# Performance work log

Hardware: AMD Instinct MI355X
Metric: run time of the kernel (lower is better)

Reference implementation:

```python
import jax, jax.numpy as jnp
import numpy as np

B = 4096          # batch
F = 1024          # feature_count * embedding_dim
E = 16            # embedding_dim (domain embedding)
D = 8             # num_domains
T = F + E         # cross-net total dim
L = 3             # cross layers
EPS = 1e-5


def setup_inputs() -> dict:
    key = jax.random.key(0)
    ks = jax.random.split(key, 32)
    s = 0.02
    inp = {}
    inp["x"] = jax.random.normal(ks[0], (B, F), dtype=jnp.float32)
    inp["domain_ids"] = jax.random.randint(ks[1], (B,), 0, D)
    # partitioned normalization params
    inp["pn_weight"] = jnp.ones((D, F), jnp.float32)
    inp["pn_bias"] = jnp.zeros((D, F), jnp.float32)
    # domain embedding table
    inp["dom_emb"] = jax.random.normal(ks[2], (D, E), jnp.float32) * 0.1
    # cross network: L layers, each Linear(T->1, no bias) + additive bias vector
    inp["cross_w"] = jax.random.normal(ks[3], (L, T), jnp.float32) * s
    inp["cross_b"] = jnp.zeros((L, T), jnp.float32)
    # center MLP: T->512->256->128 (ReLU, ReLU, none)
    inp["cW1"] = jax.random.normal(ks[4], (T, 512), jnp.float32) * s
    inp["cb1"] = jnp.zeros((512,), jnp.float32)
    inp["cW2"] = jax.random.normal(ks[5], (512, 256), jnp.float32) * s
    inp["cb2"] = jnp.zeros((256,), jnp.float32)
    inp["cW3"] = jax.random.normal(ks[6], (256, 128), jnp.float32) * s
    inp["cb3"] = jnp.zeros((128,), jnp.float32)
    # per-domain nets: T->512->256->128; last bias initialized to domain_net_init_bias=1.0
    inp["dW1"] = jax.random.normal(ks[7], (D, T, 512), jnp.float32) * s
    inp["db1"] = jnp.zeros((D, 512), jnp.float32)
    inp["dW2"] = jax.random.normal(ks[8], (D, 512, 256), jnp.float32) * s
    inp["db2"] = jnp.zeros((D, 256), jnp.float32)
    inp["dW3"] = jax.random.normal(ks[9], (D, 256, 128), jnp.float32) * s
    inp["db3"] = jnp.ones((D, 128), jnp.float32)
    # final MLP: 128->64->1
    inp["fW1"] = jax.random.normal(ks[10], (128, 64), jnp.float32) * s
    inp["fb1"] = jnp.zeros((64,), jnp.float32)
    inp["fW2"] = jax.random.normal(ks[11], (64, 1), jnp.float32) * s
    inp["fb2"] = jnp.zeros((1,), jnp.float32)
    # auxiliary net: E->32->1
    inp["aW1"] = jax.random.normal(ks[12], (E, 32), jnp.float32) * s
    inp["ab1"] = jnp.zeros((32,), jnp.float32)
    inp["aW2"] = jax.random.normal(ks[13], (32, 1), jnp.float32) * s
    inp["ab2"] = jnp.zeros((1,), jnp.float32)
    return inp


def _forward(x, domain_ids, pn_weight, pn_bias, dom_emb, cross_w, cross_b,
             cW1, cb1, cW2, cb2, cW3, cb3,
             dW1, db1, dW2, db2, dW3, db3,
             fW1, fb1, fW2, fb2, aW1, ab1, aW2, ab2):
    # --- PartitionedNormalization: per-sample LayerNorm stats + domain-indexed affine ---
    mean = jnp.mean(x, axis=1, keepdims=True)
    var = jnp.mean((x - mean) ** 2, axis=1, keepdims=True)  # unbiased=False
    normed = (x - mean) / jnp.sqrt(var + EPS)
    normed = normed * pn_weight[domain_ids] + pn_bias[domain_ids]

    xd = dom_emb[domain_ids]                    # (B, E)
    x0 = jnp.concatenate([normed, xd], axis=1)  # (B, T)

    # --- CrossNetworkWithDomain ---
    xc = x0
    for i in range(L):
        proj = xc @ cross_w[i]                  # (B,)
        xc = x0 * proj[:, None] + cross_b[i] + xc

    # --- center MLP ---
    h = jax.nn.relu(xc @ cW1 + cb1)
    h = jax.nn.relu(h @ cW2 + cb2)
    h_center = h @ cW3 + cb3                    # (B, 128)

    # --- domain-specific nets: run all D nets, select per-sample ---
    a = jax.nn.relu(jnp.einsum('bi,dio->bdo', xc, dW1) + db1[None])   # (B, D, 512)
    a = jax.nn.relu(jnp.einsum('bdi,dio->bdo', a, dW2) + db2[None])   # (B, D, 256)
    a = jnp.einsum('bdi,dio->bdo', a, dW3) + db3[None]                # (B, D, 128)
    h_domain = a[jnp.arange(a.shape[0]), domain_ids]                  # (B, 128)

    # --- STAR fusion (tanh) ---
    fused = h_center * jnp.tanh(h_domain)

    # --- final MLP + auxiliary net ---
    main_logits = jax.nn.relu(fused @ fW1 + fb1) @ fW2 + fb2          # (B, 1)
    aux_logits = jax.nn.relu(xd @ aW1 + ab1) @ aW2 + ab2              # (B, 1)
    return jax.nn.sigmoid(main_logits + aux_logits)


def reference(x, domain_ids, pn_weight, pn_bias, dom_emb, cross_w, cross_b,
              cW1, cb1, cW2, cb2, cW3, cb3,
              dW1, db1, dW2, db2, dW3, db3,
              fW1, fb1, fW2, fb2, aW1, ab1, aW2, ab2):
    return _forward(x, domain_ids, pn_weight, pn_bias, dom_emb, cross_w, cross_b,
                    cW1, cb1, cW2, cb2, cW3, cb3,
                    dW1, db1, dW2, db2, dW3, db3,
                    fW1, fb1, fW2, fb2, aW1, ab1, aW2, ab2)
```

## Files before the change

kernel.cpp:

```cpp
#include <hip/hip_runtime.h>
#include <math.h>
#include <stdint.h>

#define BATCH 4096
#define FEAT  1024
#define EDIM  16
#define NDOM  8
#define TDIM  1040
#define KP1   1088
#define NLAYER 3
#define EPSV  1e-5f

typedef __attribute__((ext_vector_type(8))) short bf16x8;
typedef __attribute__((ext_vector_type(4))) float f32x4;

__device__ __forceinline__ unsigned short f2bf(float f) {
    union { float f; unsigned int u; } v; v.f = f;
    unsigned int u = v.u;
    return (unsigned short)((u + 0x7fffu + ((u >> 16) & 1u)) >> 16);
}
__device__ __forceinline__ float bf2f(unsigned short u) {
    union { unsigned int u; float f; } v; v.u = ((unsigned int)u) << 16; return v.f;
}
__device__ __forceinline__ void gload_lds16(const void* g, void* l) {
    __builtin_amdgcn_global_load_lds(
        (const __attribute__((address_space(1))) void*)(g),
        (__attribute__((address_space(3))) void*)(l), 16, 0, 0);
}

#define T_W1 136
#define T_W2 32
#define T_W3 8
#define NCONV (T_W1*9 + T_W2*9 + T_W3*9)

__global__ __launch_bounds__(256) void front(
    const int* __restrict__ dom, int* __restrict__ perm, int* __restrict__ starts,
    const float* __restrict__ cW1, const float* __restrict__ dW1,
    const float* __restrict__ cW2, const float* __restrict__ dW2,
    const float* __restrict__ cW3, const float* __restrict__ dW3,
    unsigned short* __restrict__ Wc1b, unsigned short* __restrict__ Wd1b,
    unsigned short* __restrict__ Wc2b, unsigned short* __restrict__ Wd2b,
    unsigned short* __restrict__ Wc3b, unsigned short* __restrict__ Wd3b,
    const float* __restrict__ x,
    const float* __restrict__ pnw, const float* __restrict__ pnb,
    const float* __restrict__ demb,
    const float* __restrict__ crw, const float* __restrict__ crb,
    const float* __restrict__ aW1, const float* __restrict__ ab1,
    const float* __restrict__ aW2, const float* __restrict__ ab2,
    unsigned short* __restrict__ XCb, float* __restrict__ auxg) {
    int b = blockIdx.x;
    int t = threadIdx.x;

    if (b < NCONV) {
        __shared__ float tile[64][65];
        const float* src; unsigned short* dst; int K, N, Kp, rr;
        if (b < T_W1)            { src = cW1; dst = Wc1b; K = TDIM; N = 512; Kp = KP1; rr = b; }
        else if (b < T_W1*9)     { int r = b - T_W1; int z = r / T_W1; rr = r % T_W1;
                                   src = dW1 + (size_t)z * TDIM * 512; dst = Wd1b + (size_t)z * 512 * KP1;
                                   K = TDIM; N = 512; Kp = KP1; }
        else if (b < T_W1*9+T_W2)   { src = cW2; dst = Wc2b; K = 512; N = 256; Kp = 512; rr = b - T_W1*9; }
        else if (b < T_W1*9+T_W2*9) { int r = b - (T_W1*9+T_W2); int z = r / T_W2; rr = r % T_W2;
                                   src = dW2 + (size_t)z * 512 * 256; dst = Wd2b + (size_t)z * 256 * 512;
                                   K = 512; N = 256; Kp = 512; }
        else if (b < T_W1*9+T_W2*9+T_W3) { src = cW3; dst = Wc3b; K = 256; N = 128; Kp = 256; rr = b - (T_W1*9+T_W2*9); }
        else                     { int r = b - (T_W1*9+T_W2*9+T_W3); int z = r / T_W3; rr = r % T_W3;
                                   src = dW3 + (size_t)z * 256 * 128; dst = Wd3b + (size_t)z * 128 * 256;
                                   K = 256; N = 128; Kp = 256; }
        int kt = Kp >> 6;
        int kb = rr % kt, nb = rr / kt;
        int k0 = kb * 64, n0 = nb * 64;
        #pragma unroll
        for (int i = 0; i < 4; i++) {
            int flat = t + i * 256;
            int kr = flat >> 4, c4 = flat & 15;
            int k = k0 + kr;
            float4 v = make_float4(0.f, 0.f, 0.f, 0.f);
            if (k < K) v = *(const float4*)(src + (size_t)k * N + n0 + c4 * 4);
            tile[kr][c4 * 4 + 0] = v.x;
            tile[kr][c4 * 4 + 1] = v.y;
            tile[kr][c4 * 4 + 2] = v.z;
            tile[kr][c4 * 4 + 3] = v.w;
        }
        __syncthreads();
        #pragma unroll
        for (int i = 0; i < 4; i++) {
            int flat = t + i * 256;
            int n = flat >> 4, kg = flat & 15;
            ushort4 sv;
            sv.x = f2bf(tile[kg * 4 + 0][n]);
            sv.y = f2bf(tile[kg * 4 + 1][n]);
            sv.z = f2bf(tile[kg * 4 + 2][n]);
            sv.w = f2bf(tile[kg * 4 + 3][n]);
            *(ushort4*)(dst + (size_t)(n0 + n) * Kp + k0 + kg * 4) = sv;
        }
        return;
    }
    if (b == NCONV) {
        __shared__ int cnt[NDOM];
        __shared__ int off[NDOM];
        if (t < NDOM) cnt[t] = 0;
        __syncthreads();
        for (int i = t; i < BATCH; i += 256) atomicAdd(&cnt[dom[i]], 1);
        __syncthreads();
        if (t == 0) {
            int s = 0;
            for (int d = 0; d < NDOM; d++) { off[d] = s; starts[d] = s; s += cnt[d]; }
            starts[NDOM] = s;
        }
        __syncthreads();
        for (int i = t; i < BATCH; i += 256) {
            int p = atomicAdd(&off[dom[i]], 1);
            perm[p] = i;
        }
        return;
    }

    int w = t >> 6, lane = t & 63;
    int row = (b - NCONV - 1) * 4 + w;
    int d = dom[row];

    float4 X[4];
    #pragma unroll
    for (int j = 0; j < 4; j++)
        X[j] = *(const float4*)(x + (size_t)row * FEAT + 4 * lane + 256 * j);

    float s = 0.f, ss = 0.f;
    #pragma unroll
    for (int j = 0; j < 4; j++) {
        s  += X[j].x + X[j].y + X[j].z + X[j].w;
        ss += X[j].x*X[j].x + X[j].y*X[j].y + X[j].z*X[j].z + X[j].w*X[j].w;
    }
    #pragma unroll
    for (int m = 1; m < 64; m <<= 1) {
        s  += __shfl_xor(s,  m);
        ss += __shfl_xor(ss, m);
    }
    float mean = s / (float)FEAT;
    float var  = ss / (float)FEAT - mean * mean;
    float rstd = rsqrtf(var + EPSV);

    float4 x0[4], xc[4];
    #pragma unroll
    for (int j = 0; j < 4; j++) {
        float4 wv = *(const float4*)(pnw + (size_t)d * FEAT + 4 * lane + 256 * j);
        float4 bv = *(const float4*)(pnb + (size_t)d * FEAT + 4 * lane + 256 * j);
        x0[j].x = (X[j].x - mean) * rstd * wv.x + bv.x;
        x0[j].y = (X[j].y - mean) * rstd * wv.y + bv.y;
        x0[j].z = (X[j].z - mean) * rstd * wv.z + bv.z;
        x0[j].w = (X[j].w - mean) * rstd * wv.w + bv.w;
        xc[j] = x0[j];
    }
    float x0e = 0.f, xce = 0.f;
    if (lane < EDIM) { x0e = demb[d * EDIM + lane]; xce = x0e; }

    #pragma unroll
    for (int l = 0; l < NLAYER; l++) {
        const float* wl = crw + l * TDIM;
        const float* bl = crb + l * TDIM;
        float partial = 0.f;
        #pragma unroll
        for (int j = 0; j < 4; j++) {
            float4 wv = *(const float4*)(wl + 4 * lane + 256 * j);
            partial += xc[j].x*wv.x + xc[j].y*wv.y + xc[j].z*wv.z + xc[j].w*wv.w;
        }
        if (lane < EDIM) partial += xce * wl[FEAT + lane];
        #pragma unroll
        for (int m = 1; m < 64; m <<= 1) partial += __shfl_xor(partial, m);
        float proj = partial;
        #pragma unroll
        for (int j = 0; j < 4; j++) {
            float4 bv = *(const float4*)(bl + 4 * lane + 256 * j);
            xc[j].x = fmaf(x0[j].x, proj, bv.x + xc[j].x);
            xc[j].y = fmaf(x0[j].y, proj, bv.y + xc[j].y);
            xc[j].z = fmaf(x0[j].z, proj, bv.z + xc[j].z);
            xc[j].w = fmaf(x0[j].w, proj, bv.w + xc[j].w);
        }
        if (lane < EDIM) xce = fmaf(x0e, proj, bl[FEAT + lane] + xce);
    }

    #pragma unroll
    for (int j = 0; j < 4; j++) {
        ushort4 sv;
        sv.x = f2bf(xc[j].x); sv.y = f2bf(xc[j].y);
        sv.z = f2bf(xc[j].z); sv.w = f2bf(xc[j].w);
        *(ushort4*)(XCb + (size_t)row * KP1 + 4 * lane + 256 * j) = sv;
    }
    XCb[(size_t)row * KP1 + FEAT + lane] = (lane < EDIM) ? f2bf(xce) : 0;

    float h = (lane < 32) ? ab1[lane] : 0.f;
    #pragma unroll
    for (int e = 0; e < EDIM; e++) {
        float ev = __shfl(xce, e);
        if (lane < 32) h = fmaf(ev, aW1[e * 32 + lane], h);
    }
    float c = (lane < 32) ? fmaxf(h, 0.f) * aW2[lane] : 0.f;
    #pragma unroll
    for (int m = 1; m < 64; m <<= 1) c += __shfl_xor(c, m);
    if (lane == 0) auxg[row] = c + ab2[0];
}

__global__ __launch_bounds__(256) void gemm_mfma_v3(
    const unsigned short* __restrict__ Ac, const unsigned short* __restrict__ Ad, int lda,
    const unsigned short* __restrict__ Wc, const unsigned short* __restrict__ Wd,
    const float* __restrict__ bc, const float* __restrict__ bd,
    unsigned short* __restrict__ Cc, unsigned short* __restrict__ Cd,
    const int* __restrict__ starts, const int* __restrict__ perm, int usePerm,
    int Kp, int N, int relu) {
    __shared__ short As[128 * 64];
    __shared__ short Bs[64 * 64];

    const unsigned short* A; const unsigned short* W; const float* bias;
    unsigned short* C;
    int m0, mEnd;
    int y = blockIdx.y;
    if (y < 32) {
        A = Ac; W = Wc; bias = bc; C = Cc;
        m0 = y * 128; mEnd = BATCH;
    } else {
        int yy = y - 32;
        int d = yy >> 5, sl = yy & 31;
        int ds = starts[d], de = starts[d + 1];
        m0 = ds + sl * 128;
        if (m0 >= de) return;
        mEnd = de;
        A = Ad; W = Wd + (size_t)d * N * Kp; bias = bd + d * N; C = Cd;
    }
    int n0 = blockIdx.x * 64;
    int tid = threadIdx.x;
    int w = tid >> 6, lane = tid & 63;
    int wm = w >> 1, wn = w & 1;
    int lr = lane & 15, q = lane >> 4;

    const unsigned short* pA[4]; const unsigned short* pB[2];
    short* dA[4]; short* dB[2];
    #pragma unroll
    for (int i = 0; i < 4; i++) {
        int seg = i * 4 + w;
        int ch = seg * 64 + lane;
        int loc = ch >> 3, c = ch & 7;
        int mm = m0 + loc; if (mm > mEnd - 1) mm = mEnd - 1;
        int rowp = usePerm ? perm[mm] : mm;
        pA[i] = A + (size_t)rowp * lda + ((c ^ (loc & 7)) << 3);
        dA[i] = As + seg * 512;
    }
    #pragma unroll
    for (int i = 0; i < 2; i++) {
        int seg = i * 4 + w;
        int ch = seg * 64 + lane;
        int loc = ch >> 3, c = ch & 7;
        pB[i] = W + (size_t)(n0 + loc) * Kp + ((c ^ (loc & 7)) << 3);
        dB[i] = Bs + seg * 512;
    }

    f32x4 acc[4][2];
    #pragma unroll
    for (int i = 0; i < 4; i++)
        #pragma unroll
        for (int j = 0; j < 2; j++)
            acc[i][j] = (f32x4){0.f, 0.f, 0.f, 0.f};

    for (int k0 = 0; k0 < Kp; k0 += 64) {
        #pragma unroll
        for (int i = 0; i < 4; i++) gload_lds16(pA[i] + k0, dA[i]);
        #pragma unroll
        for (int i = 0; i < 2; i++) gload_lds16(pB[i] + k0, dB[i]);
        __syncthreads();

        #pragma unroll
        for (int half = 0; half < 2; half++) {
            int c = half * 4 + q;
            bf16x8 af[4], bf[2];
            #pragma unroll
            for (int i = 0; i < 4; i++) {
                int m = wm * 64 + i * 16 + lr;
                af[i] = *(const bf16x8*)(As + m * 64 + ((c ^ (m & 7)) << 3));
            }
            #pragma unroll
            for (int j = 0; j < 2; j++) {
                int n = wn * 32 + j * 16 + lr;
                bf[j] = *(const bf16x8*)(Bs + n * 64 + ((c ^ (n & 7)) << 3));
            }
            #pragma unroll
            for (int i = 0; i < 4; i++)
                #pragma unroll
                for (int j = 0; j < 2; j++)
                    acc[i][j] = __builtin_amdgcn_mfma_f32_16x16x32_bf16(
                        af[i], bf[j], acc[i][j], 0, 0, 0);
        }
        __syncthreads();
    }

    #pragma unroll
    for (int i = 0; i < 4; i++) {
        #pragma unroll
        for (int j = 0; j < 2; j++) {
            int col = n0 + wn * 32 + j * 16 + lr;
            float bvv = bias[col];
            int rowb = m0 + wm * 64 + i * 16 + q * 4;
            #pragma unroll
            for (int r = 0; r < 4; r++) {
                int row = rowb + r;
                if (row >= mEnd) continue;
                float val = acc[i][j][r] + bvv;
                if (relu) val = fmaxf(val, 0.f);
                C[(size_t)row * N + col] = f2bf(val);
            }
        }
    }
}

__global__ __launch_bounds__(256) void gemm3_final(
    const unsigned short* __restrict__ Ac, const unsigned short* __restrict__ Ad,
    const unsigned short* __restrict__ Wc, const unsigned short* __restrict__ Wd,
    const float* __restrict__ bc, const float* __restrict__ bd,
    const float* __restrict__ fW1, const float* __restrict__ fb1,
    const float* __restrict__ fW2, const float* __restrict__ fb2,
    const float* __restrict__ auxg, const int* __restrict__ perm,
    const int* __restrict__ starts, float* __restrict__ out) {
    __shared__ __align__(16) char smem[40960];
    short* As     = (short*)smem;
    short* Bs     = (short*)(smem + 8192);
    short* fusedB = (short*)(smem + 24576);

    int y = blockIdx.x;
    int d = y >> 6, sl = y & 63;
    int ds = starts[d], de = starts[d + 1];
    int m0 = ds + sl * 64;
    if (m0 >= de) return;
    int mEnd = de;

    int tid = threadIdx.x;
    int w = tid >> 6, lane = tid & 63;
    int wm = w >> 1, wn = w & 1;
    int lr = lane & 15, q = lane >> 4;
    const uint4 zero16 = make_uint4(0u, 0u, 0u, 0u);

    for (int chain = 0; chain < 2; chain++) {
        const unsigned short* A = chain ? Ad : Ac;
        const unsigned short* W = chain ? (Wd + (size_t)d * 128 * 256) : Wc;
        const float* bias = chain ? (bd + d * 128) : bc;
        f32x4 acc[2][4];
        #pragma unroll
        for (int i = 0; i < 2; i++)
            #pragma unroll
            for (int j = 0; j < 4; j++) acc[i][j] = (f32x4){0.f, 0.f, 0.f, 0.f};

        for (int k0 = 0; k0 < 256; k0 += 64) {
            #pragma unroll
            for (int i = 0; i < 2; i++) {
                int flat = tid + i * 256;
                int m = flat >> 3, c = flat & 7;
                int row = m0 + m;
                uint4 val = (row < mEnd)
                    ? *(const uint4*)(A + (size_t)row * 256 + k0 + c * 8) : zero16;
                *(uint4*)(As + m * 64 + ((c ^ (m & 7)) * 8)) = val;
            }
            #pragma unroll
            for (int i = 0; i < 4; i++) {
                int flat = tid + i * 256;
                int n = flat >> 3, c = flat & 7;
                uint4 val = *(const uint4*)(W + (size_t)n * 256 + k0 + c * 8);
                *(uint4*)(Bs + n * 64 + ((c ^ (n & 7)) * 8)) = val;
            }
            __syncthreads();
            #pragma unroll
            for (int g = 0; g < 2; g++) {
                int c = g * 4 + q;
                bf16x8 af[2], bf[4];
                #pragma unroll
                for (int i = 0; i < 2; i++) {
                    int m = wm * 32 + i * 16 + lr;
                    af[i] = *(const bf16x8*)(As + m * 64 + ((c ^ (m & 7)) * 8));
                }
                #pragma unroll
                for (int j = 0; j < 4; j++) {
                    int n = wn * 64 + j * 16 + lr;
                    bf[j] = *(const bf16x8*)(Bs + n * 64 + ((c ^ (n & 7)) * 8));
                }
                #pragma unroll
                for (int i = 0; i < 2; i++)
                    #pragma unroll
                    for (int j = 0; j < 4; j++)
                        acc[i][j] = __builtin_amdgcn_mfma_f32_16x16x32_bf16(
                            af[i], bf[j], acc[i][j], 0, 0, 0);
            }
            __syncthreads();
        }
        #pragma unroll
        for (int i = 0; i < 2; i++) {
            #pragma unroll
            for (int j = 0; j < 4; j++) {
                int col = wn * 64 + j * 16 + lr;
                float bvv = bias[col];
                int cch = col >> 3;
                #pragma unroll
                for (int r = 0; r < 4; r++) {
                    int row = wm * 32 + i * 16 + q * 4 + r;
                    int pc = (cch & 8) | ((cch ^ (row & 7)) & 7);
                    int idx = row * 128 + pc * 8 + (col & 7);
                    if (chain == 0) {
                        fusedB[idx] = (short)f2bf(acc[i][j][r] + bvv);
                    } else {
                        float cv = bf2f((unsigned short)fusedB[idx]);
                        fusedB[idx] = (short)f2bf(cv * tanhf(acc[i][j][r] + bvv));
                    }
                }
            }
        }
    }
    __syncthreads();

    short* Bsf = Bs;
    float* Ls  = (float*)As;
    for (int s2 = tid; s2 < 1024; s2 += 256) {
        int n = s2 >> 4, cch = s2 & 15;
        bf16x8 vv;
        #pragma unroll
        for (int kk = 0; kk < 8; kk++)
            vv[kk] = (short)f2bf(fW1[(cch * 8 + kk) * 64 + n]);
        int pc = (cch & 8) | ((cch ^ (n & 7)) & 7);
        *(bf16x8*)(Bsf + n * 128 + pc * 8) = vv;
    }
    __syncthreads();

    f32x4 acc2[2][2];
    #pragma unroll
    for (int i = 0; i < 2; i++)
        #pragma unroll
        for (int j = 0; j < 2; j++) acc2[i][j] = (f32x4){0.f, 0.f, 0.f, 0.f};
    #pragma unroll
    for (int g = 0; g < 4; g++) {
        int c = g * 4 + q;
        bf16x8 af[2], bf[2];
        #pragma unroll
        for (int i = 0; i < 2; i++) {
            int m = wm * 32 + i * 16 + lr;
            int pc = (c & 8) | ((c ^ (m & 7)) & 7);
            af[i] = *(const bf16x8*)(fusedB + m * 128 + pc * 8);
        }
        #pragma unroll
        for (int j = 0; j < 2; j++) {
            int n = wn * 32 + j * 16 + lr;
            int pc = (c & 8) | ((c ^ (n & 7)) & 7);
            bf[j] = *(const bf16x8*)(Bsf + n * 128 + pc * 8);
        }
        #pragma unroll
        for (int i = 0; i < 2; i++)
            #pragma unroll
            for (int j = 0; j < 2; j++)
                acc2[i][j] = __builtin_amdgcn_mfma_f32_16x16x32_bf16(
                    af[i], bf[j], acc2[i][j], 0, 0, 0);
    }

    float w2v[2], b1v[2];
    #pragma unroll
    for (int j = 0; j < 2; j++) {
        int col = wn * 32 + j * 16 + lr;
        w2v[j] = fW2[col];
        b1v[j] = fb1[col];
    }
    float rowv[2][4];
    #pragma unroll
    for (int i = 0; i < 2; i++)
        #pragma unroll
        for (int r = 0; r < 4; r++) {
            float v = 0.f;
            #pragma unroll
            for (int j = 0; j < 2; j++)
                v += fmaxf(acc2[i][j][r] + b1v[j], 0.f) * w2v[j];
            v += __shfl_xor(v, 1);
            v += __shfl_xor(v, 2);
            v += __shfl_xor(v, 4);
            v += __shfl_xor(v, 8);
            rowv[i][r] = v;
        }
    if (wn == 0 && lr == 0) {
        #pragma unroll
        for (int i = 0; i < 2; i++)
            #pragma unroll
            for (int r = 0; r < 4; r++)
                Ls[wm * 32 + i * 16 + q * 4 + r] = rowv[i][r];
    }
    __syncthreads();
    if (wn == 1 && lr == 0) {
        float b2 = fb2[0];
        #pragma unroll
        for (int i = 0; i < 2; i++)
            #pragma unroll
            for (int r = 0; r < 4; r++) {
                int row = wm * 32 + i * 16 + q * 4 + r;
                int p = m0 + row;
                if (p < mEnd) {
                    int orow = perm[p];
                    float logit = Ls[row] + rowv[i][r] + b2 + auxg[orow];
                    out[orow] = 1.f / (1.f + expf(-logit));
                }
            }
    }
}

extern "C" void kernel_launch(void* const* d_in, const int* in_sizes, int n_in,
                              void* d_out, int out_size, void* d_ws, size_t ws_size,
                              hipStream_t stream) {
    (void)in_sizes; (void)n_in; (void)out_size; (void)ws_size;

    const float* x    = (const float*)d_in[0];
    const int*   dom  = (const int*)  d_in[1];
    const float* pnw  = (const float*)d_in[2];
    const float* pnb  = (const float*)d_in[3];
    const float* demb = (const float*)d_in[4];
    const float* crw  = (const float*)d_in[5];
    const float* crb  = (const float*)d_in[6];
    const float* cW1  = (const float*)d_in[7];
    const float* cb1  = (const float*)d_in[8];
    const float* cW2  = (const float*)d_in[9];
    const float* cb2  = (const float*)d_in[10];
    const float* cW3  = (const float*)d_in[11];
    const float* cb3  = (const float*)d_in[12];
    const float* dW1  = (const float*)d_in[13];
    const float* db1  = (const float*)d_in[14];
    const float* dW2  = (const float*)d_in[15];
    const float* db2  = (const float*)d_in[16];
    const float* dW3  = (const float*)d_in[17];
    const float* db3  = (const float*)d_in[18];
    const float* fW1  = (const float*)d_in[19];
    const float* fb1  = (const float*)d_in[20];
    const float* fW2  = (const float*)d_in[21];
    const float* fb2  = (const float*)d_in[22];
    const float* aW1  = (const float*)d_in[23];
    const float* ab1  = (const float*)d_in[24];
    const float* aW2  = (const float*)d_in[25];
    const float* ab2  = (const float*)d_in[26];
    float* out = (float*)d_out;

    char* base = (char*)d_ws;
    size_t o = 0;
    auto alloc = [&](size_t bytes) { char* p = base + o; o += (bytes + 255) & ~size_t(255); return p; };

    int* perm   = (int*)alloc(BATCH * 4);
    int* starts = (int*)alloc((NDOM + 1) * 4);
    float* auxg = (float*)alloc(BATCH * 4);
    unsigned short* XCb  = (unsigned short*)alloc((size_t)BATCH * KP1 * 2);
    unsigned short* H1c  = (unsigned short*)alloc((size_t)BATCH * 512 * 2);
    unsigned short* H1d  = (unsigned short*)alloc((size_t)BATCH * 512 * 2);
    unsigned short* H2c  = (unsigned short*)alloc((size_t)BATCH * 256 * 2);
    unsigned short* H2d  = (unsigned short*)alloc((size_t)BATCH * 256 * 2);
    unsigned short* Wc1b = (unsigned short*)alloc((size_t)512 * KP1 * 2);
    unsigned short* Wd1b = (unsigned short*)alloc((size_t)NDOM * 512 * KP1 * 2);
    unsigned short* Wc2b = (unsigned short*)alloc((size_t)256 * 512 * 2);
    unsigned short* Wd2b = (unsigned short*)alloc((size_t)NDOM * 256 * 512 * 2);
    unsigned short* Wc3b = (unsigned short*)alloc((size_t)128 * 256 * 2);
    unsigned short* Wd3b = (unsigned short*)alloc((size_t)NDOM * 128 * 256 * 2);

    front<<<NCONV + 1 + BATCH / 4, 256, 0, stream>>>(
        dom, perm, starts, cW1, dW1, cW2, dW2, cW3, dW3,
        Wc1b, Wd1b, Wc2b, Wd2b, Wc3b, Wd3b,
        x, pnw, pnb, demb, crw, crb, aW1, ab1, aW2, ab2, XCb, auxg);

    gemm_mfma_v3<<<dim3(512 / 64, 32 + NDOM * 32), 256, 0, stream>>>(
        XCb, XCb, KP1, Wc1b, Wd1b, cb1, db1, H1c, H1d, starts, perm, 1, KP1, 512, 1);
    gemm_mfma_v3<<<dim3(256 / 64, 32 + NDOM * 32), 256, 0, stream>>>(
        H1c, H1d, 512, Wc2b, Wd2b, cb2, db2, H2c, H2d, starts, perm, 0, 512, 256, 1);

    gemm3_final<<<NDOM * 64, 256, 0, stream>>>(
        H2c, H2d, Wc3b, Wd3b, cb3, db3, fW1, fb1, fW2, fb2,
        auxg, perm, starts, out);
}
```

Measured before the change: 216.7 us.

## Use smaller row tiles for layer-2 GEMM and final fused kernel

Adds a new GEMM kernel with 64x64 tiles and async global-to-LDS loads for the second MLP layer, replacing the larger-tile v3 launch. The final fused kernel (layer 3, tanh fusion, final MLP) now processes 32 rows per block instead of 64, with a smaller LDS footprint. The aim is more blocks in flight across the many CUs for these small GEMMs. In exchange, weight tiles are reloaded more often per row. The per-domain grid also assumes no domain has more than 1024 rows in the layer-2 kernel.

```diff
diff --git a/kernel.cpp b/kernel.cpp
--- a/kernel.cpp
+++ b/kernel.cpp
@@ -309,6 +309,109 @@
     }
 }
 
+__global__ __launch_bounds__(256) void gemm_mfma_v4(
+    const unsigned short* __restrict__ Ac, const unsigned short* __restrict__ Ad, int lda,
+    const unsigned short* __restrict__ Wc, const unsigned short* __restrict__ Wd,
+    const float* __restrict__ bc, const float* __restrict__ bd,
+    unsigned short* __restrict__ Cc, unsigned short* __restrict__ Cd,
+    const int* __restrict__ starts,
+    int Kp, int N, int relu) {
+    __shared__ short As[64 * 64];
+    __shared__ short Bs[64 * 64];
+
+    const unsigned short* A; const unsigned short* W; const float* bias;
+    unsigned short* C;
+    int m0, mEnd;
+    int y = blockIdx.y;
+    if (y < 64) {
+        A = Ac; W = Wc; bias = bc; C = Cc;
+        m0 = y * 64; mEnd = BATCH;
+    } else {
+        int yy = y - 64;
+        int d = yy >> 4, sl = yy & 15;
+        int ds = starts[d], de = starts[d + 1];
+        m0 = ds + sl * 64;
+        if (m0 >= de) return;
+        mEnd = de;
+        A = Ad; W = Wd + (size_t)d * N * Kp; bias = bd + d * N; C = Cd;
+    }
+    int n0 = blockIdx.x * 64;
+    int tid = threadIdx.x;
+    int w = tid >> 6, lane = tid & 63;
+    int wm = w >> 1, wn = w & 1;
+    int lr = lane & 15, q = lane >> 4;
+
+    const unsigned short* pA[2]; const unsigned short* pB[2];
+    short* dA[2]; short* dB[2];
+    #pragma unroll
+    for (int i = 0; i < 2; i++) {
+        int seg = i * 4 + w;
+        int ch = seg * 64 + lane;
+        int loc = ch >> 3, c = ch & 7;
+        int mm = m0 + loc; if (mm > mEnd - 1) mm = mEnd - 1;
+        pA[i] = A + (size_t)mm * lda + ((c ^ (loc & 7)) << 3);
+        dA[i] = As + seg * 512;
+        pB[i] = W + (size_t)(n0 + loc) * Kp + ((c ^ (loc & 7)) << 3);
+        dB[i] = Bs + seg * 512;
+    }
+
+    f32x4 acc[2][2];
+    #pragma unroll
+    for (int i = 0; i < 2; i++)
+        #pragma unroll
+        for (int j = 0; j < 2; j++)
+            acc[i][j] = (f32x4){0.f, 0.f, 0.f, 0.f};
+
+    for (int k0 = 0; k0 < Kp; k0 += 64) {
+        #pragma unroll
+        for (int i = 0; i < 2; i++) gload_lds16(pA[i] + k0, dA[i]);
+        #pragma unroll
+        for (int i = 0; i < 2; i++) gload_lds16(pB[i] + k0, dB[i]);
+        __syncthreads();
+
+        #pragma unroll
+        for (int half = 0; half < 2; half++) {
+            int c = half * 4 + q;
+            bf16x8 af[2], bf[2];
+            #pragma unroll
+            for (int i = 0; i < 2; i++) {
+                int m = wm * 32 + i * 16 + lr;
+                af[i] = *(const bf16x8*)(As + m * 64 + ((c ^ (m & 7)) << 3));
+            }
+            #pragma unroll
+            for (int j = 0; j < 2; j++) {
+                int n = wn * 32 + j * 16 + lr;
+                bf[j] = *(const bf16x8*)(Bs + n * 64 + ((c ^ (n & 7)) << 3));
+            }
+            #pragma unroll
+            for (int i = 0; i < 2; i++)
+                #pragma unroll
+                for (int j = 0; j < 2; j++)
+                    acc[i][j] = __builtin_amdgcn_mfma_f32_16x16x32_bf16(
+                        af[i], bf[j], acc[i][j], 0, 0, 0);
+        }
+        __syncthreads();
+    }
+
+    #pragma unroll
+    for (int i = 0; i < 2; i++) {
+        #pragma unroll
+        for (int j = 0; j < 2; j++) {
+            int col = n0 + wn * 32 + j * 16 + lr;
+            float bvv = bias[col];
+            int rowb = m0 + wm * 32 + i * 16 + q * 4;
+            #pragma unroll
+            for (int r = 0; r < 4; r++) {
+                int row = rowb + r;
+                if (row >= mEnd) continue;
+                float val = acc[i][j][r] + bvv;
+                if (relu) val = fmaxf(val, 0.f);
+                C[(size_t)row * N + col] = f2bf(val);
+            }
+        }
+    }
+}
+
 __global__ __launch_bounds__(256) void gemm3_final(
     const unsigned short* __restrict__ Ac, const unsigned short* __restrict__ Ad,
     const unsigned short* __restrict__ Wc, const unsigned short* __restrict__ Wd,
@@ -317,15 +420,15 @@
     const float* __restrict__ fW2, const float* __restrict__ fb2,
     const float* __restrict__ auxg, const int* __restrict__ perm,
     const int* __restrict__ starts, float* __restrict__ out) {
-    __shared__ __align__(16) char smem[40960];
-    short* As     = (short*)smem;
-    short* Bs     = (short*)(smem + 8192);
-    short* fusedB = (short*)(smem + 24576);
+    __shared__ __align__(16) char smem[28672];
+    short* As    = (short*)smem;
+    short* Bs    = (short*)(smem + 4096);
+    short* fused = (short*)(smem + 20480);
 
     int y = blockIdx.x;
-    int d = y >> 6, sl = y & 63;
+    int d = y >> 7, sl = y & 127;
     int ds = starts[d], de = starts[d + 1];
-    int m0 = ds + sl * 64;
+    int m0 = ds + sl * 32;
     if (m0 >= de) return;
     int mEnd = de;
 
@@ -339,17 +442,13 @@
         const unsigned short* A = chain ? Ad : Ac;
         const unsigned short* W = chain ? (Wd + (size_t)d * 128 * 256) : Wc;
         const float* bias = chain ? (bd + d * 128) : bc;
-        f32x4 acc[2][4];
-        #pragma unroll
-        for (int i = 0; i < 2; i++)
-            #pragma unroll
-            for (int j = 0; j < 4; j++) acc[i][j] = (f32x4){0.f, 0.f, 0.f, 0.f};
+        f32x4 acc[4];
+        #pragma unroll
+        for (int j = 0; j < 4; j++) acc[j] = (f32x4){0.f, 0.f, 0.f, 0.f};
 
         for (int k0 = 0; k0 < 256; k0 += 64) {
-            #pragma unroll
-            for (int i = 0; i < 2; i++) {
-                int flat = tid + i * 256;
-                int m = flat >> 3, c = flat & 7;
+            {
+                int m = tid >> 3, c = tid & 7;
                 int row = m0 + m;
                 uint4 val = (row < mEnd)
                     ? *(const uint4*)(A + (size_t)row * 256 + k0 + c * 8) : zero16;
@@ -366,49 +465,37 @@
             #pragma unroll
             for (int g = 0; g < 2; g++) {
                 int c = g * 4 + q;
-                bf16x8 af[2], bf[4];
-                #pragma unroll
-                for (int i = 0; i < 2; i++) {
-                    int m = wm * 32 + i * 16 + lr;
-                    af[i] = *(const bf16x8*)(As + m * 64 + ((c ^ (m & 7)) * 8));
-                }
+                int m = wm * 16 + lr;
+                bf16x8 af = *(const bf16x8*)(As + m * 64 + ((c ^ (m & 7)) * 8));
                 #pragma unroll
                 for (int j = 0; j < 4; j++) {
                     int n = wn * 64 + j * 16 + lr;
-                    bf[j] = *(const bf16x8*)(Bs + n * 64 + ((c ^ (n & 7)) * 8));
+                    bf16x8 bf = *(const bf16x8*)(Bs + n * 64 + ((c ^ (n & 7)) * 8));
+                    acc[j] = __builtin_amdgcn_mfma_f32_16x16x32_bf16(af, bf, acc[j], 0, 0, 0);
                 }
-                #pragma unroll
-                for (int i = 0; i < 2; i++)
-                    #pragma unroll
-                    for (int j = 0; j < 4; j++)
-                        acc[i][j] = __builtin_amdgcn_mfma_f32_16x16x32_bf16(
-                            af[i], bf[j], acc[i][j], 0, 0, 0);
             }
             __syncthreads();
         }
         #pragma unroll
-        for (int i = 0; i < 2; i++) {
-            #pragma unroll
-            for (int j = 0; j < 4; j++) {
-                int col = wn * 64 + j * 16 + lr;
-                float bvv = bias[col];
-                int cch = col >> 3;
-                #pragma unroll
-                for (int r = 0; r < 4; r++) {
-                    int row = wm * 32 + i * 16 + q * 4 + r;
-                    int pc = (cch & 8) | ((cch ^ (row & 7)) & 7);
-                    int idx = row * 128 + pc * 8 + (col & 7);
-                    if (chain == 0) {
-                        fusedB[idx] = (short)f2bf(acc[i][j][r] + bvv);
-                    } else {
-                        float cv = bf2f((unsigned short)fusedB[idx]);
-                        fusedB[idx] = (short)f2bf(cv * tanhf(acc[i][j][r] + bvv));
-                    }
+        for (int j = 0; j < 4; j++) {
+            int col = wn * 64 + j * 16 + lr;
+            float bvv = bias[col];
+            int cch = col >> 3;
+            #pragma unroll
+            for (int r = 0; r < 4; r++) {
+                int row = wm * 16 + q * 4 + r;
+                int pc = (cch & 8) | ((cch ^ (row & 7)) & 7);
+                int idx = row * 128 + pc * 8 + (col & 7);
+                if (chain == 0) {
+                    fused[idx] = (short)f2bf(acc[j][r] + bvv);
+                } else {
+                    float cv = bf2f((unsigned short)fused[idx]);
+                    fused[idx] = (short)f2bf(cv * tanhf(acc[j][r] + bvv));
                 }
             }
         }
-    }
-    __syncthreads();
+        __syncthreads();
+    }
 
     short* Bsf = Bs;
     float* Ls  = (float*)As;
@@ -423,33 +510,22 @@
     }
     __syncthreads();
 
-    f32x4 acc2[2][2];
-    #pragma unroll
-    for (int i = 0; i < 2; i++)
-        #pragma unroll
-        for (int j = 0; j < 2; j++) acc2[i][j] = (f32x4){0.f, 0.f, 0.f, 0.f};
+    f32x4 acc2[2];
+    #pragma unroll
+    for (int j = 0; j < 2; j++) acc2[j] = (f32x4){0.f, 0.f, 0.f, 0.f};
     #pragma unroll
     for (int g = 0; g < 4; g++) {
         int c = g * 4 + q;
-        bf16x8 af[2], bf[2];
-        #pragma unroll
-        for (int i = 0; i < 2; i++) {
-            int m = wm * 32 + i * 16 + lr;
-            int pc = (c & 8) | ((c ^ (m & 7)) & 7);
-            af[i] = *(const bf16x8*)(fusedB + m * 128 + pc * 8);
-        }
+        int m = wm * 16 + lr;
+        int pcm = (c & 8) | ((c ^ (m & 7)) & 7);
+        bf16x8 af = *(const bf16x8*)(fused + m * 128 + pcm * 8);
         #pragma unroll
         for (int j = 0; j < 2; j++) {
             int n = wn * 32 + j * 16 + lr;
-            int pc = (c & 8) | ((c ^ (n & 7)) & 7);
-            bf[j] = *(const bf16x8*)(Bsf + n * 128 + pc * 8);
-        }
-        #pragma unroll
-        for (int i = 0; i < 2; i++)
-            #pragma unroll
-            for (int j = 0; j < 2; j++)
-                acc2[i][j] = __builtin_amdgcn_mfma_f32_16x16x32_bf16(
-                    af[i], bf[j], acc2[i][j], 0, 0, 0);
+            int pcn = (c & 8) | ((c ^ (n & 7)) & 7);
+            bf16x8 bf = *(const bf16x8*)(Bsf + n * 128 + pcn * 8);
+            acc2[j] = __builtin_amdgcn_mfma_f32_16x16x32_bf16(af, bf, acc2[j], 0, 0, 0);
+        }
     }
 
     float w2v[2], b1v[2];
@@ -459,43 +535,37 @@
         w2v[j] = fW2[col];
         b1v[j] = fb1[col];
     }
-    float rowv[2][4];
-    #pragma unroll
-    for (int i = 0; i < 2; i++)
-        #pragma unroll
-        for (int r = 0; r < 4; r++) {
-            float v = 0.f;
-            #pragma unroll
-            for (int j = 0; j < 2; j++)
-                v += fmaxf(acc2[i][j][r] + b1v[j], 0.f) * w2v[j];
-            v += __shfl_xor(v, 1);
-            v += __shfl_xor(v, 2);
-            v += __shfl_xor(v, 4);
-            v += __shfl_xor(v, 8);
-            rowv[i][r] = v;
-        }
+    float rowv[4];
+    #pragma unroll
+    for (int r = 0; r < 4; r++) {
+        float v = 0.f;
+        #pragma unroll
+        for (int j = 0; j < 2; j++)
+            v += fmaxf(acc2[j][r] + b1v[j], 0.f) * w2v[j];
+        v += __shfl_xor(v, 1);
+        v += __shfl_xor(v, 2);
+        v += __shfl_xor(v, 4);
+        v += __shfl_xor(v, 8);
+        rowv[r] = v;
+    }
     if (wn == 0 && lr == 0) {
         #pragma unroll
-        for (int i = 0; i < 2; i++)
-            #pragma unroll
-            for (int r = 0; r < 4; r++)
-                Ls[wm * 32 + i * 16 + q * 4 + r] = rowv[i][r];
+        for (int r = 0; r < 4; r++)
+            Ls[wm * 16 + q * 4 + r] = rowv[r];
     }
     __syncthreads();
     if (wn == 1 && lr == 0) {
         float b2 = fb2[0];
         #pragma unroll
-        for (int i = 0; i < 2; i++)
-            #pragma unroll
-            for (int r = 0; r < 4; r++) {
-                int row = wm * 32 + i * 16 + q * 4 + r;
-                int p = m0 + row;
-                if (p < mEnd) {
-                    int orow = perm[p];
-                    float logit = Ls[row] + rowv[i][r] + b2 + auxg[orow];
-                    out[orow] = 1.f / (1.f + expf(-logit));
-                }
-            }
+        for (int r = 0; r < 4; r++) {
+            int row = wm * 16 + q * 4 + r;
+            int p = m0 + row;
+            if (p < mEnd) {
+                int orow = perm[p];
+                float logit = Ls[row] + rowv[r] + b2 + auxg[orow];
+                out[orow] = 1.f / (1.f + expf(-logit));
+            }
+        }
     }
 }
 
@@ -559,10 +629,10 @@
 
     gemm_mfma_v3<<<dim3(512 / 64, 32 + NDOM * 32), 256, 0, stream>>>(
         XCb, XCb, KP1, Wc1b, Wd1b, cb1, db1, H1c, H1d, starts, perm, 1, KP1, 512, 1);
-    gemm_mfma_v3<<<dim3(256 / 64, 32 + NDOM * 32), 256, 0, stream>>>(
-        H1c, H1d, 512, Wc2b, Wd2b, cb2, db2, H2c, H2d, starts, perm, 0, 512, 256, 1);
-
-    gemm3_final<<<NDOM * 64, 256, 0, stream>>>(
+    gemm_mfma_v4<<<dim3(256 / 64, 64 + NDOM * 16), 256, 0, stream>>>(
+        H1c, H1d, 512, Wc2b, Wd2b, cb2, db2, H2c, H2d, starts, 512, 256, 1);
+
+    gemm3_final<<<NDOM * 128, 256, 0, stream>>>(
         H2c, H2d, Wc3b, Wd3b, cb3, db3, fW1, fb1, fW2, fb2,
         auxg, perm, starts, out);
 }
```

New measurement: 205.7 us. -5.1%, faster.
